# Kernel optimization log

Measured on AMD Instinct MI355X. Metric: run time of the kernel, lower is better.

## Reference

```python
import jax, jax.numpy as jnp
import numpy as np

CUT_SIZE = 224
CUTN = 128
SIDE = 1024
CUT_POW = 1.0


def setup_inputs() -> dict:
    key = jax.random.key(0)
    x = jax.random.uniform(key, (1, 3, SIDE, SIDE), dtype=jnp.float32)
    rng = np.random.default_rng(0)
    max_size = SIDE
    min_size = min(SIDE, SIDE, CUT_SIZE)
    r = rng.random(CUTN)
    sizes = (r ** CUT_POW * (max_size - min_size) + min_size).astype(np.int32)
    oy = np.array([rng.integers(0, SIDE - int(s) + 1) for s in sizes], dtype=np.int32)
    ox = np.array([rng.integers(0, SIDE - int(s) + 1) for s in sizes], dtype=np.int32)
    return {
        "input": x,
        "sizes": jnp.asarray(sizes),
        "offsety": jnp.asarray(oy),
        "offsetx": jnp.asarray(ox),
    }


def _cutout(img, size, oy, ox):
    # img: [B, C, H, W]; crop a size x size window at (oy, ox) and bilinearly
    # resample to CUT_SIZE x CUT_SIZE (align_corners=False convention).
    H, W = img.shape[2], img.shape[3]
    scale = size.astype(jnp.float32) / CUT_SIZE
    coords = (jnp.arange(CUT_SIZE, dtype=jnp.float32) + 0.5) * scale - 0.5
    ys = jnp.clip(oy.astype(jnp.float32) + coords, 0.0, H - 1.0)
    xs = jnp.clip(ox.astype(jnp.float32) + coords, 0.0, W - 1.0)
    y0 = jnp.floor(ys).astype(jnp.int32)
    x0 = jnp.floor(xs).astype(jnp.int32)
    y1 = jnp.minimum(y0 + 1, H - 1)
    x1 = jnp.minimum(x0 + 1, W - 1)
    wy = (ys - y0.astype(jnp.float32))[None, None, :, None]
    wx = (xs - x0.astype(jnp.float32))[None, None, None, :]
    # separable bilinear: interpolate rows, then columns
    rows = img[:, :, y0, :] * (1.0 - wy) + img[:, :, y1, :] * wy  # [B,C,cs,W]
    out = rows[:, :, :, x0] * (1.0 - wx) + rows[:, :, :, x1] * wx  # [B,C,cs,cs]
    return out


def _make_cutouts(input, sizes, offsety, offsetx):
    cuts = jax.vmap(_cutout, in_axes=(None, 0, 0, 0))(input, sizes, offsety, offsetx)
    # [cutn, B, C, cs, cs] -> torch.cat(dim=0) layout [cutn*B, C, cs, cs]
    n, b, c, h, w = cuts.shape
    return cuts.reshape(n * b, c, h, w)


def reference(input, sizes, offsety, offsetx):
    out = _make_cutouts(input, sizes, offsety, offsetx)
    # ClampWithGrad forward is a plain clamp
    return jnp.clip(out, 0.0, 1.0)
```

## Files before the change

kernel.cpp:

```cpp
#include <hip/hip_runtime.h>
#include <hip/hip_fp16.h>

#define CUT_SIZE 224
#define SIDE 1024
#define CUTN 128
#define NSLAB 8
#define SLAB_BLOCKS 192
#define SLAB_WSLOTS (SLAB_BLOCKS * 4)
#define LDSW2 1032

#define WS_A     0
#define WS_B     (NSLAB * CUTN)
#define WS_TOT   (2 * NSLAB * CUTN)
#define WS_WORDS (2 * NSLAB * CUTN + NSLAB)

__global__ __launch_bounds__(256) void plan_kernel(
    const int* __restrict__ sizes, const int* __restrict__ offy,
    unsigned int* __restrict__ ws)
{
    __shared__ float s_inv[CUTN], s_oy[CUTN];
    __shared__ int   s_wt[CUTN];
    __shared__ int   cdf[129];
    __shared__ int   qb[NSLAB + 1];
    __shared__ unsigned short slen[NSLAB][CUTN];
    const int t = threadIdx.x;

    if (t < CUTN) {
        const int sz = sizes[t];
        s_inv[t] = (float)CUT_SIZE / (float)sz;
        s_oy[t]  = (float)offy[t];
        s_wt[t]  = 200 + (sz >> 2);
    }
    __syncthreads();

    for (int k = t; k <= 128; k += 256) {
        const float Yf = (float)(k << 3);
        int c = 0;
        for (int n = 0; n < CUTN; ++n) {
            const float thr = (Yf + 0.5f - s_oy[n]) * s_inv[n] - 0.5f;
            c += min(CUT_SIZE, max(0, (int)ceilf(thr))) * s_wt[n];
        }
        cdf[k] = c;
    }
    __syncthreads();

    if (t >= 1 && t < NSLAB) {
        const long long target = (long long)t * (long long)cdf[128] / NSLAB;
        int lo = 0, hi = 128;
        while (hi - lo > 1) { const int m = (lo + hi) >> 1;
                              if ((long long)cdf[m] >= target) hi = m; else lo = m; }
        qb[t] = hi << 3;
    }
    if (t == 0) { qb[0] = 0; qb[NSLAB] = SIDE; }
    __syncthreads();

    for (int idx = t; idx < NSLAB * CUTN; idx += 256) {
        const int s = idx >> 7, n = idx & (CUTN - 1);
        int rlo, rhi;
        { const int Y = qb[s];
          rlo = (Y <= 0) ? 0
              : min(CUT_SIZE, max(0, (int)ceilf(((float)Y + 0.5f - s_oy[n]) * s_inv[n] - 0.5f))); }
        { const int Y = qb[s + 1];
          rhi = (Y >= SIDE) ? CUT_SIZE
              : min(CUT_SIZE, max(0, (int)ceilf(((float)Y + 0.5f - s_oy[n]) * s_inv[n] - 0.5f))); }
        slen[s][n] = (unsigned short)(rhi - rlo);
        ws[WS_B + idx] = (unsigned)rlo;
    }
    __syncthreads();

    if (t < NSLAB) {
        unsigned run = 0;
        for (int n = 0; n < CUTN; ++n) {
            ws[WS_A + t * CUTN + n] = run;
            run += slen[t][n];
        }
        ws[WS_TOT + t] = run;
    }
}

__global__ __launch_bounds__(256) void cutout_row_kernel(
    const float* __restrict__ img,
    const int* __restrict__ sizes,
    const int* __restrict__ offy,
    const int* __restrict__ offx,
    const unsigned int* __restrict__ ws,
    float* __restrict__ out)
{
    __shared__ __half lds[4][3][LDSW2];
    const int s    = blockIdx.x & 7;
    const int w    = threadIdx.x >> 6;
    const int lane = threadIdx.x & 63;
    const unsigned q = (unsigned)(blockIdx.x >> 3) * 4u + (unsigned)w;

    const unsigned* __restrict__ A = ws + WS_A + s * CUTN;
    const unsigned* __restrict__ B = ws + WS_B + s * CUTN;
    const unsigned T = ws[WS_TOT + s];
    __half* __restrict__ l0 = &lds[w][0][0];
    __half* __restrict__ l1 = &lds[w][1][0];
    __half* __restrict__ l2 = &lds[w][2][0];

    const unsigned aLo = A[lane],            aHi = A[64 + lane];
    const unsigned bLo = B[lane],            bHi = B[64 + lane];
    const float   szLo = (float)sizes[lane], szHi = (float)sizes[64 + lane];
    const float   oyLo = (float)offy[lane],  oyHi = (float)offy[64 + lane];
    const float   oxLo = (float)offx[lane],  oxHi = (float)offx[64 + lane];

    for (unsigned i = q; i < T; i += SLAB_WSLOTS) {
        int n = 0;
        unsigned An = 0;
#pragma unroll
        for (int st = 64; st; st >>= 1) {
            const int m = n | st;
            const unsigned Am = (m & 64) ? (unsigned)__shfl((int)aHi, m & 63)
                                         : (unsigned)__shfl((int)aLo, m & 63);
            if (Am <= i) { n = m; An = Am; }
        }
        const int hi6 = n & 64, lo6 = n & 63;
        const unsigned rlo = hi6 ? (unsigned)__shfl((int)bHi, lo6)
                                 : (unsigned)__shfl((int)bLo, lo6);
        const int   y  = (int)rlo + (int)(i - An);
        const float sz = hi6 ? __shfl(szHi, lo6) : __shfl(szLo, lo6);
        const float oy = hi6 ? __shfl(oyHi, lo6) : __shfl(oyLo, lo6);
        const float ox = hi6 ? __shfl(oxHi, lo6) : __shfl(oxLo, lo6);

        const float scale = sz * (1.0f / (float)CUT_SIZE);

        float fy = fmaf((float)y + 0.5f, scale, oy - 0.5f);
        fy = fminf(fmaxf(fy, 0.0f), (float)(SIDE - 1));
        const int   y0 = (int)fy;
        const int   y1 = min(y0 + 1, SIDE - 1);
        const float wy  = fy - (float)y0;
        const float wy0 = 1.0f - wy;

        float fx0 = fmaf(0.5f, scale, ox - 0.5f);
        fx0 = fminf(fmaxf(fx0, 0.0f), (float)(SIDE - 1));
        float fxl = fmaf((float)CUT_SIZE - 0.5f, scale, ox - 0.5f);
        fxl = fminf(fmaxf(fxl, 0.0f), (float)(SIDE - 1));
        const int xb    = (int)fx0;
        const int xe    = min((int)fxl + 1, SIDE - 1);
        const int xb4   = xb & ~3;
        const int ilast = xe - xb4;
        const int nf4   = (ilast >> 2) + 1;

        const size_t cstride = (size_t)SIDE * SIDE;
        const float* b0 = img + (size_t)y0 * SIDE + xb4;
        const float* b1 = img + (size_t)y1 * SIDE + xb4;
        const float4* __restrict__ rp0 = reinterpret_cast<const float4*>(b0);
        const float4* __restrict__ rq0 = reinterpret_cast<const float4*>(b1);
        const float4* __restrict__ rp1 = reinterpret_cast<const float4*>(b0 + cstride);
        const float4* __restrict__ rq1 = reinterpret_cast<const float4*>(b1 + cstride);
        const float4* __restrict__ rp2 = reinterpret_cast<const float4*>(b0 + 2 * cstride);
        const float4* __restrict__ rq2 = reinterpret_cast<const float4*>(b1 + 2 * cstride);

        for (int k = lane; k < nf4; k += 64) {
            const float4 a0 = rp0[k], c0 = rq0[k];
            const float4 a1 = rp1[k], c1 = rq1[k];
            const float4 a2 = rp2[k], c2 = rq2[k];
            union { __half2 h[2]; uint2 u; } pk;
            pk.h[0] = __floats2half2_rn(a0.x * wy0 + c0.x * wy, a0.y * wy0 + c0.y * wy);
            pk.h[1] = __floats2half2_rn(a0.z * wy0 + c0.z * wy, a0.w * wy0 + c0.w * wy);
            *reinterpret_cast<uint2*>(l0 + 4 * k) = pk.u;
            pk.h[0] = __floats2half2_rn(a1.x * wy0 + c1.x * wy, a1.y * wy0 + c1.y * wy);
            pk.h[1] = __floats2half2_rn(a1.z * wy0 + c1.z * wy, a1.w * wy0 + c1.w * wy);
            *reinterpret_cast<uint2*>(l1 + 4 * k) = pk.u;
            pk.h[0] = __floats2half2_rn(a2.x * wy0 + c2.x * wy, a2.y * wy0 + c2.y * wy);
            pk.h[1] = __floats2half2_rn(a2.z * wy0 + c2.z * wy, a2.w * wy0 + c2.w * wy);
            *reinterpret_cast<uint2*>(l2 + 4 * k) = pk.u;
        }
        if (lane < 3) (&lds[w][lane][0])[ilast + 1] = __float2half(0.0f);
        asm volatile("s_waitcnt lgkmcnt(0)" ::: "memory");

        const int p0 = lane << 2;
        if (p0 < CUT_SIZE) {
            const float xb4f = (float)xb4;
            float fx = fmaf((float)p0 + 0.5f, scale, ox - 0.5f);
            float4 o0, o1, o2;
            float* v0 = &o0.x; float* v1 = &o1.x; float* v2 = &o2.x;
#pragma unroll
            for (int j = 0; j < 4; ++j) {
                const float fxj = fminf(fmaxf(fx, 0.0f), (float)(SIDE - 1));
                fx += scale;
                const float fl = fxj - xb4f;
                const int   i0 = (int)fl;
                const float wx  = fl - (float)i0;
                const float wx0 = 1.0f - wx;
                v0[j] = fminf(fmaxf(__half2float(l0[i0]) * wx0 + __half2float(l0[i0 + 1]) * wx, 0.0f), 1.0f);
                v1[j] = fminf(fmaxf(__half2float(l1[i0]) * wx0 + __half2float(l1[i0 + 1]) * wx, 0.0f), 1.0f);
                v2[j] = fminf(fmaxf(__half2float(l2[i0]) * wx0 + __half2float(l2[i0 + 1]) * wx, 0.0f), 1.0f);
            }
            const size_t obase = (((size_t)n * 3) * CUT_SIZE + y) * CUT_SIZE + p0;
            *reinterpret_cast<float4*>(out + obase) = o0;
            *reinterpret_cast<float4*>(out + obase + CUT_SIZE * CUT_SIZE) = o1;
            *reinterpret_cast<float4*>(out + obase + 2 * (CUT_SIZE * CUT_SIZE)) = o2;
        }
        asm volatile("" ::: "memory");
    }
}

__global__ __launch_bounds__(128) void make_cutouts_fallback(
    const float* __restrict__ img, const int* __restrict__ sizes,
    const int* __restrict__ offy, const int* __restrict__ offx,
    float* __restrict__ out)
{
    __shared__ float lds[2][1032];
    const int n    = blockIdx.y;
    const int w    = threadIdx.x >> 6;
    const int lane = threadIdx.x & 63;
    const int y    = blockIdx.x * 2 + w;
    const float scale = (float)sizes[n] * (1.0f / (float)CUT_SIZE);
    const float oy = (float)offy[n];
    const float ox = (float)offx[n];
    float fy = fmaf((float)y + 0.5f, scale, oy - 0.5f);
    fy = fminf(fmaxf(fy, 0.0f), (float)(SIDE - 1));
    const int y0 = (int)fy, y1 = min(y0 + 1, SIDE - 1);
    const float wy = fy - (float)y0, wy0 = 1.0f - wy;
    float fx0 = fmaf(0.5f, scale, ox - 0.5f);
    fx0 = fminf(fmaxf(fx0, 0.0f), (float)(SIDE - 1));
    float fxl = fmaf((float)CUT_SIZE - 0.5f, scale, ox - 0.5f);
    fxl = fminf(fmaxf(fxl, 0.0f), (float)(SIDE - 1));
    const int xb = (int)fx0, xe = min((int)fxl + 1, SIDE - 1);
    const int xb4 = xb & ~3, ilast = xe - xb4, nf4 = (ilast >> 2) + 1;
    int i0r[4], i1r[4]; float wxr[4], wx0r[4];
#pragma unroll
    for (int it = 0; it < 4; ++it) {
        const int p = min(lane + it * 64, CUT_SIZE - 1);
        float fx = fmaf((float)p + 0.5f, scale, ox - 0.5f);
        fx = fminf(fmaxf(fx, 0.0f), (float)(SIDE - 1));
        const float fl = fx - (float)xb4;
        const int i0 = (int)fl;
        i0r[it] = i0; i1r[it] = min(i0 + 1, ilast);
        wxr[it] = fl - (float)i0; wx0r[it] = 1.0f - wxr[it];
    }
    const int r0off = y0 * SIDE + xb4, r1off = y1 * SIDE + xb4;
    float* __restrict__ l = lds[w];
    const size_t obase0 = (((size_t)n * 3) * CUT_SIZE + y) * CUT_SIZE;
    for (int c = 0; c < 3; ++c) {
        const float* __restrict__ ch = img + (size_t)c * (SIDE * SIDE);
        const float4* __restrict__ rp0 = reinterpret_cast<const float4*>(ch + r0off);
        const float4* __restrict__ rp1 = reinterpret_cast<const float4*>(ch + r1off);
        for (int k = lane; k < nf4; k += 64) {
            const float4 a = rp0[k]; const float4 b = rp1[k];
            float4 r;
            r.x = a.x * wy0 + b.x * wy; r.y = a.y * wy0 + b.y * wy;
            r.z = a.z * wy0 + b.z * wy; r.w = a.w * wy0 + b.w * wy;
            *reinterpret_cast<float4*>(l + 4 * k) = r;
        }
        asm volatile("s_waitcnt lgkmcnt(0)" ::: "memory");
        const size_t obase = obase0 + (size_t)c * (CUT_SIZE * CUT_SIZE);
#pragma unroll
        for (int it = 0; it < 4; ++it) {
            const int p = lane + it * 64;
            if (p < CUT_SIZE) {
                float v = l[i0r[it]] * wx0r[it] + l[i1r[it]] * wxr[it];
                v = fminf(fmaxf(v, 0.0f), 1.0f);
                out[obase + p] = v;
            }
        }
        asm volatile("" ::: "memory");
    }
}

extern "C" void kernel_launch(void* const* d_in, const int* in_sizes, int n_in,
                              void* d_out, int out_size, void* d_ws, size_t ws_size,
                              hipStream_t stream) {
    const float* img   = (const float*)d_in[0];
    const int*   sizes = (const int*)d_in[1];
    const int*   offy  = (const int*)d_in[2];
    const int*   offx  = (const int*)d_in[3];
    float*       out   = (float*)d_out;

    if (ws_size >= (size_t)WS_WORDS * 4) {
        unsigned int* ws = (unsigned int*)d_ws;
        plan_kernel<<<1, 256, 0, stream>>>(sizes, offy, ws);
        cutout_row_kernel<<<NSLAB * SLAB_BLOCKS, 256, 0, stream>>>(
            img, sizes, offy, offx, ws, out);
    } else {
        make_cutouts_fallback<<<dim3(CUT_SIZE / 2, CUTN), 128, 0, stream>>>(
            img, sizes, offy, offx, out);
    }
}
```

Measured before the change: 40.42 us.

## Fuse slab planning into the cutout kernel, recomputing the plan per block

Removes the separate single-block plan kernel and its workspace round trip. Each of the 1536 blocks now recomputes the slab CDF, the slab boundaries and a per-slab prefix scan in shared memory before resampling. This saves one launch and its dependency, but adds redundant per-block setup work (129 threads each looping over 128 cuts, plus a log-step scan with barriers). The cost-weight constant also changes from 200 to 100, which shifts how rows are balanced across slabs.

```diff
diff --git a/kernel.cpp b/kernel.cpp
--- a/kernel.cpp
+++ b/kernel.cpp
@@ -9,101 +9,94 @@
 #define SLAB_WSLOTS (SLAB_BLOCKS * 4)
 #define LDSW2 1032
 
-#define WS_A     0
-#define WS_B     (NSLAB * CUTN)
-#define WS_TOT   (2 * NSLAB * CUTN)
-#define WS_WORDS (2 * NSLAB * CUTN + NSLAB)
-
-__global__ __launch_bounds__(256) void plan_kernel(
-    const int* __restrict__ sizes, const int* __restrict__ offy,
-    unsigned int* __restrict__ ws)
-{
-    __shared__ float s_inv[CUTN], s_oy[CUTN];
-    __shared__ int   s_wt[CUTN];
-    __shared__ int   cdf[129];
-    __shared__ int   qb[NSLAB + 1];
-    __shared__ unsigned short slen[NSLAB][CUTN];
-    const int t = threadIdx.x;
-
-    if (t < CUTN) {
-        const int sz = sizes[t];
-        s_inv[t] = (float)CUT_SIZE / (float)sz;
-        s_oy[t]  = (float)offy[t];
-        s_wt[t]  = 200 + (sz >> 2);
-    }
-    __syncthreads();
-
-    for (int k = t; k <= 128; k += 256) {
-        const float Yf = (float)(k << 3);
-        int c = 0;
-        for (int n = 0; n < CUTN; ++n) {
-            const float thr = (Yf + 0.5f - s_oy[n]) * s_inv[n] - 0.5f;
-            c += min(CUT_SIZE, max(0, (int)ceilf(thr))) * s_wt[n];
-        }
-        cdf[k] = c;
-    }
-    __syncthreads();
-
-    if (t >= 1 && t < NSLAB) {
-        const long long target = (long long)t * (long long)cdf[128] / NSLAB;
-        int lo = 0, hi = 128;
-        while (hi - lo > 1) { const int m = (lo + hi) >> 1;
-                              if ((long long)cdf[m] >= target) hi = m; else lo = m; }
-        qb[t] = hi << 3;
-    }
-    if (t == 0) { qb[0] = 0; qb[NSLAB] = SIDE; }
-    __syncthreads();
-
-    for (int idx = t; idx < NSLAB * CUTN; idx += 256) {
-        const int s = idx >> 7, n = idx & (CUTN - 1);
-        int rlo, rhi;
-        { const int Y = qb[s];
-          rlo = (Y <= 0) ? 0
-              : min(CUT_SIZE, max(0, (int)ceilf(((float)Y + 0.5f - s_oy[n]) * s_inv[n] - 0.5f))); }
-        { const int Y = qb[s + 1];
-          rhi = (Y >= SIDE) ? CUT_SIZE
-              : min(CUT_SIZE, max(0, (int)ceilf(((float)Y + 0.5f - s_oy[n]) * s_inv[n] - 0.5f))); }
-        slen[s][n] = (unsigned short)(rhi - rlo);
-        ws[WS_B + idx] = (unsigned)rlo;
-    }
-    __syncthreads();
-
-    if (t < NSLAB) {
-        unsigned run = 0;
-        for (int n = 0; n < CUTN; ++n) {
-            ws[WS_A + t * CUTN + n] = run;
-            run += slen[t][n];
-        }
-        ws[WS_TOT + t] = run;
-    }
-}
-
-__global__ __launch_bounds__(256) void cutout_row_kernel(
+__global__ __launch_bounds__(256) void cutout_fused_kernel(
     const float* __restrict__ img,
     const int* __restrict__ sizes,
     const int* __restrict__ offy,
     const int* __restrict__ offx,
-    const unsigned int* __restrict__ ws,
     float* __restrict__ out)
 {
     __shared__ __half lds[4][3][LDSW2];
     const int s    = blockIdx.x & 7;
     const int w    = threadIdx.x >> 6;
     const int lane = threadIdx.x & 63;
+    const int t    = threadIdx.x;
     const unsigned q = (unsigned)(blockIdx.x >> 3) * 4u + (unsigned)w;
 
-    const unsigned* __restrict__ A = ws + WS_A + s * CUTN;
-    const unsigned* __restrict__ B = ws + WS_B + s * CUTN;
-    const unsigned T = ws[WS_TOT + s];
+    float* pf  = reinterpret_cast<float*>(&lds[0][0][0]);
+    int*   pi  = reinterpret_cast<int*>(&lds[0][0][0]);
+    float* fInv = pf;
+    float* fOy  = pf + 128;
+    int*   iWt  = pi + 256;
+    int*   cdf  = pi + 384;
+    int*   qbv  = pi + 513;
+    int*   lenv = pi + 522;
+    int*   rlov = pi + 650;
+    int*   scv  = pi + 778;
+
+    if (t < CUTN) {
+        const int sz = sizes[t];
+        fInv[t] = (float)CUT_SIZE / (float)sz;
+        fOy[t]  = (float)offy[t];
+        iWt[t]  = 100 + (sz >> 2);
+    }
+    __syncthreads();
+
+    if (t <= 128) {
+        const float Yf = (float)(t << 3);
+        int c = 0;
+        for (int n = 0; n < CUTN; ++n) {
+            const float thr = (Yf + 0.5f - fOy[n]) * fInv[n] - 0.5f;
+            c += min(CUT_SIZE, max(0, (int)ceilf(thr))) * iWt[n];
+        }
+        cdf[t] = c;
+    }
+    __syncthreads();
+
+    if (t >= 1 && t < NSLAB) {
+        const long long target = (long long)t * (long long)cdf[128] / NSLAB;
+        int lo = 0, hi = 128;
+        while (hi - lo > 1) { const int m = (lo + hi) >> 1;
+                              if ((long long)cdf[m] >= target) hi = m; else lo = m; }
+        qbv[t] = hi << 3;
+    }
+    if (t == 0) { qbv[0] = 0; qbv[NSLAB] = SIDE; }
+    __syncthreads();
+
+    if (t < CUTN) {
+        int rlo, rhi;
+        { const int Y = qbv[s];
+          rlo = (Y <= 0) ? 0
+              : min(CUT_SIZE, max(0, (int)ceilf(((float)Y + 0.5f - fOy[t]) * fInv[t] - 0.5f))); }
+        { const int Y = qbv[s + 1];
+          rhi = (Y >= SIDE) ? CUT_SIZE
+              : min(CUT_SIZE, max(0, (int)ceilf(((float)Y + 0.5f - fOy[t]) * fInv[t] - 0.5f))); }
+        rlov[t] = rlo;
+        lenv[t] = rhi - rlo;
+        scv[t]  = rhi - rlo;
+    }
+    __syncthreads();
+    for (int off = 1; off < CUTN; off <<= 1) {
+        int v = 0;
+        if (t < CUTN && t >= off) v = scv[t - off];
+        __syncthreads();
+        if (t < CUTN) scv[t] += v;
+        __syncthreads();
+    }
+
+    const unsigned aLo = (unsigned)(scv[lane]      - lenv[lane]);
+    const unsigned aHi = (unsigned)(scv[64 + lane] - lenv[64 + lane]);
+    const unsigned bLo = (unsigned)rlov[lane];
+    const unsigned bHi = (unsigned)rlov[64 + lane];
+    const unsigned T   = (unsigned)scv[CUTN - 1];
+    const float   szLo = (float)sizes[lane], szHi = (float)sizes[64 + lane];
+    const float   oyLo = (float)offy[lane],  oyHi = (float)offy[64 + lane];
+    const float   oxLo = (float)offx[lane],  oxHi = (float)offx[64 + lane];
+    __syncthreads();
+
     __half* __restrict__ l0 = &lds[w][0][0];
     __half* __restrict__ l1 = &lds[w][1][0];
     __half* __restrict__ l2 = &lds[w][2][0];
-
-    const unsigned aLo = A[lane],            aHi = A[64 + lane];
-    const unsigned bLo = B[lane],            bHi = B[64 + lane];
-    const float   szLo = (float)sizes[lane], szHi = (float)sizes[64 + lane];
-    const float   oyLo = (float)offy[lane],  oyHi = (float)offy[64 + lane];
-    const float   oxLo = (float)offx[lane],  oxHi = (float)offx[64 + lane];
 
     for (unsigned i = q; i < T; i += SLAB_WSLOTS) {
         int n = 0;
@@ -197,69 +190,6 @@
     }
 }
 
-__global__ __launch_bounds__(128) void make_cutouts_fallback(
-    const float* __restrict__ img, const int* __restrict__ sizes,
-    const int* __restrict__ offy, const int* __restrict__ offx,
-    float* __restrict__ out)
-{
-    __shared__ float lds[2][1032];
-    const int n    = blockIdx.y;
-    const int w    = threadIdx.x >> 6;
-    const int lane = threadIdx.x & 63;
-    const int y    = blockIdx.x * 2 + w;
-    const float scale = (float)sizes[n] * (1.0f / (float)CUT_SIZE);
-    const float oy = (float)offy[n];
-    const float ox = (float)offx[n];
-    float fy = fmaf((float)y + 0.5f, scale, oy - 0.5f);
-    fy = fminf(fmaxf(fy, 0.0f), (float)(SIDE - 1));
-    const int y0 = (int)fy, y1 = min(y0 + 1, SIDE - 1);
-    const float wy = fy - (float)y0, wy0 = 1.0f - wy;
-    float fx0 = fmaf(0.5f, scale, ox - 0.5f);
-    fx0 = fminf(fmaxf(fx0, 0.0f), (float)(SIDE - 1));
-    float fxl = fmaf((float)CUT_SIZE - 0.5f, scale, ox - 0.5f);
-    fxl = fminf(fmaxf(fxl, 0.0f), (float)(SIDE - 1));
-    const int xb = (int)fx0, xe = min((int)fxl + 1, SIDE - 1);
-    const int xb4 = xb & ~3, ilast = xe - xb4, nf4 = (ilast >> 2) + 1;
-    int i0r[4], i1r[4]; float wxr[4], wx0r[4];
-#pragma unroll
-    for (int it = 0; it < 4; ++it) {
-        const int p = min(lane + it * 64, CUT_SIZE - 1);
-        float fx = fmaf((float)p + 0.5f, scale, ox - 0.5f);
-        fx = fminf(fmaxf(fx, 0.0f), (float)(SIDE - 1));
-        const float fl = fx - (float)xb4;
-        const int i0 = (int)fl;
-        i0r[it] = i0; i1r[it] = min(i0 + 1, ilast);
-        wxr[it] = fl - (float)i0; wx0r[it] = 1.0f - wxr[it];
-    }
-    const int r0off = y0 * SIDE + xb4, r1off = y1 * SIDE + xb4;
-    float* __restrict__ l = lds[w];
-    const size_t obase0 = (((size_t)n * 3) * CUT_SIZE + y) * CUT_SIZE;
-    for (int c = 0; c < 3; ++c) {
-        const float* __restrict__ ch = img + (size_t)c * (SIDE * SIDE);
-        const float4* __restrict__ rp0 = reinterpret_cast<const float4*>(ch + r0off);
-        const float4* __restrict__ rp1 = reinterpret_cast<const float4*>(ch + r1off);
-        for (int k = lane; k < nf4; k += 64) {
-            const float4 a = rp0[k]; const float4 b = rp1[k];
-            float4 r;
-            r.x = a.x * wy0 + b.x * wy; r.y = a.y * wy0 + b.y * wy;
-            r.z = a.z * wy0 + b.z * wy; r.w = a.w * wy0 + b.w * wy;
-            *reinterpret_cast<float4*>(l + 4 * k) = r;
-        }
-        asm volatile("s_waitcnt lgkmcnt(0)" ::: "memory");
-        const size_t obase = obase0 + (size_t)c * (CUT_SIZE * CUT_SIZE);
-#pragma unroll
-        for (int it = 0; it < 4; ++it) {
-            const int p = lane + it * 64;
-            if (p < CUT_SIZE) {
-                float v = l[i0r[it]] * wx0r[it] + l[i1r[it]] * wxr[it];
-                v = fminf(fmaxf(v, 0.0f), 1.0f);
-                out[obase + p] = v;
-            }
-        }
-        asm volatile("" ::: "memory");
-    }
-}
-
 extern "C" void kernel_launch(void* const* d_in, const int* in_sizes, int n_in,
                               void* d_out, int out_size, void* d_ws, size_t ws_size,
                               hipStream_t stream) {
@@ -269,13 +199,6 @@
     const int*   offx  = (const int*)d_in[3];
     float*       out   = (float*)d_out;
 
-    if (ws_size >= (size_t)WS_WORDS * 4) {
-        unsigned int* ws = (unsigned int*)d_ws;
-        plan_kernel<<<1, 256, 0, stream>>>(sizes, offy, ws);
-        cutout_row_kernel<<<NSLAB * SLAB_BLOCKS, 256, 0, stream>>>(
-            img, sizes, offy, offx, ws, out);
-    } else {
-        make_cutouts_fallback<<<dim3(CUT_SIZE / 2, CUTN), 128, 0, stream>>>(
-            img, sizes, offy, offx, out);
-    }
+    cutout_fused_kernel<<<NSLAB * SLAB_BLOCKS, 256, 0, stream>>>(
+        img, sizes, offy, offx, out);
 }
```

Result: faster. 38.53 us (median of 2 runs) (-4.7%).
